# Performance work log

Hardware: AMD Instinct MI355X
Metric: run time of the kernel (lower is better)

## Reference

```python
import jax, jax.numpy as jnp
import numpy as np

B, NC, CN, K, DN = 2, 256, 256, 16, 64
G, HM, HS, HMOD, MOD_OUT = 8, 128, 128, 64, 5


def setup_inputs() -> dict:
    rng = np.random.default_rng(0)
    # per-neuron top-K neighbors within cell, excluding self, sorted (matches torch buffer build)
    scores = rng.random((NC, CN, CN)).astype(np.float32)
    ii = np.arange(CN)
    scores[:, ii, ii] = -np.inf
    conn = np.argpartition(-scores, K, axis=-1)[..., :K]
    conn = np.sort(conn, axis=-1).astype(np.int32)  # [NC, CN, K]

    key = jax.random.key(0)
    ks = jax.random.split(key, 12)
    n = lambda k, s, sc=1.0: jax.random.normal(k, s, jnp.float32) * sc
    return {
        'h': n(ks[0], (B, NC, CN, DN), 0.01),
        'w_conn': n(ks[1], (B, NC, CN, K), 0.1),
        'cell_context': n(ks[2], (B, NC, DN), 0.1),
        'neuron_id': n(ks[3], (NC, CN, DN), 0.02),
        'msg_w1': n(ks[4], (G, HM, 3 * DN), 0.05), 'msg_b1': jnp.zeros((G, HM)),
        'msg_w2': n(ks[5], (G, DN, HM), 0.005), 'msg_b2': jnp.zeros((G, DN)),
        'state_w1': n(ks[6], (G, HS, 3 * DN), 0.05), 'state_b1': jnp.zeros((G, HS)),
        'state_w2': n(ks[7], (G, DN, HS), 0.005), 'state_b2': jnp.zeros((G, DN)),
        'mod_w1': n(ks[8], (NC, 2 * DN, HMOD), 0.05), 'mod_b1': jnp.zeros((NC, HMOD)),
        'mod_w2': n(ks[9], (NC, HMOD, MOD_OUT), 0.0005), 'mod_b2': jnp.zeros((NC, MOD_OUT)),
        'conn_idx': jnp.asarray(conn),
        'cell_to_group': (jnp.arange(NC) % G).astype(jnp.int32),
    }


def reference(h, w_conn, cell_context, neuron_id,
              msg_w1, msg_b1, msg_w2, msg_b2,
              state_w1, state_b1, state_w2, state_b2,
              mod_w1, mod_b1, mod_w2, mod_b2,
              conn_idx, cell_to_group):
    nc = h.shape[1]
    cell_ix = jnp.arange(nc)[:, None, None]
    # gather K-neighbor states per neuron: [B, NC, CN, K, DN]
    nb = jax.vmap(lambda hb: hb[cell_ix, conn_idx])(h)
    # connection-weighted aggregation
    agg = jnp.einsum('bnck,bnckd->bncd', w_conn, nb)

    g = cell_to_group  # [NC]
    # grouped message MLP (2-layer), per-cell weights gathered from group table
    mfeat = jnp.concatenate([h, agg, jnp.broadcast_to(neuron_id[None], h.shape)], axis=-1)
    mh = jax.nn.gelu(jnp.einsum('bncf,nhf->bnch', mfeat, msg_w1[g]) + msg_b1[g][None, :, None, :])
    msg = jnp.einsum('bnch,ndh->bncd', mh, msg_w2[g]) + msg_b2[g][None, :, None, :]

    # grouped state MLP, residual update on h
    ctx = jnp.broadcast_to(cell_context[:, :, None, :], h.shape)
    sfeat = jnp.concatenate([h, msg, ctx], axis=-1)
    sh = jax.nn.gelu(jnp.einsum('bncf,nhf->bnch', sfeat, state_w1[g]) + state_b1[g][None, :, None, :])
    h_new = h + jnp.einsum('bnch,ndh->bncd', sh, state_w2[g]) + state_b2[g][None, :, None, :]

    # per-cell modulation MLP on pooled stats (h_mean || msg_mean)
    pooled = jnp.concatenate([h_new.mean(axis=2), msg.mean(axis=2)], axis=-1)  # [B, NC, 2DN]
    ph = jax.nn.gelu(jnp.einsum('bnf,nfh->bnh', pooled, mod_w1) + mod_b1[None])
    mod = jnp.einsum('bnh,nho->bno', ph, mod_w2) + mod_b2[None]
    return h_new, msg, mod
```

## Files before the change

kernel.cpp:

```cpp
#include <hip/hip_runtime.h>

#define B_   2
#define NC_  256
#define CN_  256
#define K_   16
#define DN_  64
#define G_   8
#define HM_  128
#define F3_  192

typedef unsigned short u16;
typedef short v8s __attribute__((ext_vector_type(8)));
typedef float v4f __attribute__((ext_vector_type(4)));

#define SMEM_BYTES 150144


__device__ __forceinline__ u16 f2b(float f) {
    unsigned v; __builtin_memcpy(&v, &f, 4);
    v = v + 0x7fffu + ((v >> 16) & 1u);
    return (u16)(v >> 16);
}
__device__ __forceinline__ v8s cvt8(const float* p) {
    float4 a = *(const float4*)p, b = *(const float4*)(p + 4);
    v8s r;
    r[0] = (short)f2b(a.x); r[1] = (short)f2b(a.y); r[2] = (short)f2b(a.z); r[3] = (short)f2b(a.w);
    r[4] = (short)f2b(b.x); r[5] = (short)f2b(b.y); r[6] = (short)f2b(b.z); r[7] = (short)f2b(b.w);
    return r;
}
__device__ __forceinline__ float gelu_t(float x) {
    float u = x * x;
    float t = 1.5957691216057308f * x * __builtin_fmaf(0.044715f, u, 1.0f);
    float e = __expf(-t);
    return x * __builtin_amdgcn_rcpf(1.0f + e);
}

__global__ __launch_bounds__(256) void cvt_w(
    const float* __restrict__ mw1, const float* __restrict__ mw2,
    const float* __restrict__ sw1, const float* __restrict__ sw2,
    u16* __restrict__ dst)
{
    int e = (blockIdx.x * 256 + threadIdx.x) * 4;
    const float* s; int off;
    if      (e < 196608) { s = mw1; off = e; }
    else if (e < 262144) { s = mw2; off = e - 196608; }
    else if (e < 458752) { s = sw1; off = e - 262144; }
    else                 { s = sw2; off = e - 458752; }
    float4 v = *(const float4*)(s + off);
    ushort4 o4;
    o4.x = f2b(v.x); o4.y = f2b(v.y); o4.z = f2b(v.z); o4.w = f2b(v.w);
    *(ushort4*)(dst + e) = o4;
}

__global__ __launch_bounds__(256) void mg_main(
    const float* __restrict__ h,    const float* __restrict__ wconn,
    const float* __restrict__ ctx,  const float* __restrict__ nid,
    const u16* __restrict__ mw1b,   const float* __restrict__ mb1,
    const u16* __restrict__ mw2b,   const float* __restrict__ mb2,
    const u16* __restrict__ sw1b,   const float* __restrict__ sb1,
    const u16* __restrict__ sw2b,   const float* __restrict__ sb2,
    const int* __restrict__ conn,   const int* __restrict__ c2g,
    const float* __restrict__ dw1,  const float* __restrict__ db1,
    const float* __restrict__ dw2,  const float* __restrict__ db2,
    float* __restrict__ outf)
{
    const int bn   = blockIdx.x;
    const int n    = bn & 255;
    const int tid  = threadIdx.x;
    const int wave = tid >> 6;
    const int lane = tid & 63;
    const int q    = lane >> 4;
    const int ln   = lane & 15;
    const int g    = c2g[n];

    extern __shared__ char smem[];
    u16*   hT   = (u16*)(smem);
    u16*   big  = (u16*)(smem + 34816);
    u16*   wg   = big;
    u16*   am   = (u16*)(smem + 104448);
    u16*   ctxl = (u16*)(smem + 141312);
    float* hsum = (float*)(smem + 141440);
    float* msum = (float*)(smem + 145536);
    float* pool = (float*)(smem + 149632);

    const size_t hbase = (size_t)bn * (CN_ * DN_);
    const size_t nbase = (size_t)n  * (CN_ * DN_);
    float* oH = outf + (size_t)bn * 16384;
    float* oM = outf + (size_t)8388608 + (size_t)bn * 16384;

    if (tid < 64) ctxl[tid] = f2b(ctx[(size_t)bn * DN_ + tid]);
    {
        const float* hrow = h + hbase + (size_t)tid * DN_;
#pragma unroll
        for (int i = 0; i < 16; ++i) {
            float4 v = *(const float4*)(hrow + i * 4);
            hT[(i * 4 + 0) * 272 + tid] = f2b(v.x);
            hT[(i * 4 + 1) * 272 + tid] = f2b(v.y);
            hT[(i * 4 + 2) * 272 + tid] = f2b(v.z);
            hT[(i * 4 + 3) * 272 + tid] = f2b(v.w);
        }
    }
    __syncthreads();

    for (int s = 0; s < 4; ++s) {
#pragma unroll
        for (int i = 0; i < 9; ++i) {
            int idx = tid + i * 256;
            if (idx < 2176) ((uint4*)wg)[idx] = make_uint4(0u, 0u, 0u, 0u);
        }
        __syncthreads();
#pragma unroll
        for (int i = 0; i < 4; ++i) {
            int p  = i * 256 + tid;
            int cl = p >> 4;
            int iv = conn[n * 4096 + s * 1024 + p];
            float wv = wconn[(size_t)bn * 4096 + s * 1024 + p];
            wg[cl * 272 + iv] = f2b(wv);
        }
        __syncthreads();
        {
            v4f a0 = {0,0,0,0}, a1 = {0,0,0,0}, a2 = {0,0,0,0}, a3 = {0,0,0,0};
            const u16* arow = wg + (wave * 16 + ln) * 272 + q * 8;
#pragma unroll
            for (int ks = 0; ks < 8; ++ks) {
                v8s a   = *(const v8s*)(arow + ks * 32);
                v8s bb0 = *(const v8s*)(hT + ( 0 + ln) * 272 + ks * 32 + q * 8);
                v8s bb1 = *(const v8s*)(hT + (16 + ln) * 272 + ks * 32 + q * 8);
                v8s bb2 = *(const v8s*)(hT + (32 + ln) * 272 + ks * 32 + q * 8);
                v8s bb3 = *(const v8s*)(hT + (48 + ln) * 272 + ks * 32 + q * 8);
                a0 = __builtin_amdgcn_mfma_f32_16x16x32_bf16(a, bb0, a0, 0, 0, 0);
                a1 = __builtin_amdgcn_mfma_f32_16x16x32_bf16(a, bb1, a1, 0, 0, 0);
                a2 = __builtin_amdgcn_mfma_f32_16x16x32_bf16(a, bb2, a2, 0, 0, 0);
                a3 = __builtin_amdgcn_mfma_f32_16x16x32_bf16(a, bb3, a3, 0, 0, 0);
            }
            int crow = s * 64 + wave * 16 + q * 4;
#pragma unroll
            for (int r = 0; r < 4; ++r) {
                am[(crow + r) * 72 +  0 + ln] = f2b(a0[r]);
                am[(crow + r) * 72 + 16 + ln] = f2b(a1[r]);
                am[(crow + r) * 72 + 32 + ln] = f2b(a2[r]);
                am[(crow + r) * 72 + 48 + ln] = f2b(a3[r]);
            }
        }
        __syncthreads();
    }

    const int cbase = wave * 64;

    {
        v8s afr[4][6];
#pragma unroll
        for (int mi = 0; mi < 4; ++mi) {
            int c = cbase + mi * 16 + ln;
            afr[mi][0] = cvt8(h + hbase + (size_t)c * 64 +  0 + q * 8);
            afr[mi][1] = cvt8(h + hbase + (size_t)c * 64 + 32 + q * 8);
            afr[mi][2] = *(const v8s*)(am + c * 72 +  0 + q * 8);
            afr[mi][3] = *(const v8s*)(am + c * 72 + 32 + q * 8);
            afr[mi][4] = cvt8(nid + nbase + (size_t)c * 64 +  0 + q * 8);
            afr[mi][5] = cvt8(nid + nbase + (size_t)c * 64 + 32 + q * 8);
        }
        float b1v[8];
#pragma unroll
        for (int nt = 0; nt < 8; ++nt) b1v[nt] = mb1[g * HM_ + nt * 16 + ln];
        const u16* w1g = mw1b + (size_t)g * HM_ * F3_;
#pragma unroll
        for (int nt = 0; nt < 8; ++nt) {
            v4f acc[4] = {{0,0,0,0},{0,0,0,0},{0,0,0,0},{0,0,0,0}};
#pragma unroll
            for (int ks = 0; ks < 6; ++ks) {
                v8s bf = *(const v8s*)(w1g + (nt * 16 + ln) * F3_ + ks * 32 + q * 8);
#pragma unroll
                for (int mi = 0; mi < 4; ++mi)
                    acc[mi] = __builtin_amdgcn_mfma_f32_16x16x32_bf16(afr[mi][ks], bf, acc[mi], 0, 0, 0);
            }
#pragma unroll
            for (int mi = 0; mi < 4; ++mi) {
                int c = cbase + mi * 16 + q * 4;
#pragma unroll
                for (int r = 0; r < 4; ++r)
                    big[(c + r) * 136 + nt * 16 + ln] = f2b(gelu_t(acc[mi][r] + b1v[nt]));
            }
        }
    }

    {
        v8s afr[4][4];
#pragma unroll
        for (int mi = 0; mi < 4; ++mi) {
            int c = cbase + mi * 16 + ln;
#pragma unroll
            for (int ks = 0; ks < 4; ++ks)
                afr[mi][ks] = *(const v8s*)(big + c * 136 + ks * 32 + q * 8);
        }
        const u16* w2g = mw2b + (size_t)g * DN_ * HM_;
        float mpart[4];
#pragma unroll
        for (int nt = 0; nt < 4; ++nt) {
            float bb = mb2[g * DN_ + nt * 16 + ln];
            v4f acc[4] = {{0,0,0,0},{0,0,0,0},{0,0,0,0},{0,0,0,0}};
#pragma unroll
            for (int ks = 0; ks < 4; ++ks) {
                v8s bf = *(const v8s*)(w2g + (nt * 16 + ln) * HM_ + ks * 32 + q * 8);
#pragma unroll
                for (int mi = 0; mi < 4; ++mi)
                    acc[mi] = __builtin_amdgcn_mfma_f32_16x16x32_bf16(afr[mi][ks], bf, acc[mi], 0, 0, 0);
            }
            float ms = 0.0f;
            int d = nt * 16 + ln;
#pragma unroll
            for (int mi = 0; mi < 4; ++mi) {
                int c = cbase + mi * 16 + q * 4;
#pragma unroll
                for (int r = 0; r < 4; ++r) {
                    float mv = acc[mi][r] + bb;
                    am[(c + r) * 72 + d] = f2b(mv);
                    oM[(size_t)(c + r) * 64 + d] = mv;
                    ms += mv;
                }
            }
            mpart[nt] = ms;
        }
#pragma unroll
        for (int nt = 0; nt < 4; ++nt)
            msum[(wave * 4 + q) * 64 + nt * 16 + ln] = mpart[nt];
    }

    {
        v8s cfr0 = *(const v8s*)(ctxl +  0 + q * 8);
        v8s cfr1 = *(const v8s*)(ctxl + 32 + q * 8);
        v8s afr[4][4];
#pragma unroll
        for (int mi = 0; mi < 4; ++mi) {
            int c = cbase + mi * 16 + ln;
            afr[mi][0] = cvt8(h + hbase + (size_t)c * 64 +  0 + q * 8);
            afr[mi][1] = cvt8(h + hbase + (size_t)c * 64 + 32 + q * 8);
            afr[mi][2] = *(const v8s*)(am + c * 72 +  0 + q * 8);
            afr[mi][3] = *(const v8s*)(am + c * 72 + 32 + q * 8);
        }
        float b1v[8];
#pragma unroll
        for (int nt = 0; nt < 8; ++nt) b1v[nt] = sb1[g * HM_ + nt * 16 + ln];
        const u16* w1g = sw1b + (size_t)g * HM_ * F3_;
#pragma unroll
        for (int nt = 0; nt < 8; ++nt) {
            v4f acc[4] = {{0,0,0,0},{0,0,0,0},{0,0,0,0},{0,0,0,0}};
#pragma unroll
            for (int ks = 0; ks < 4; ++ks) {
                v8s bf = *(const v8s*)(w1g + (nt * 16 + ln) * F3_ + ks * 32 + q * 8);
#pragma unroll
                for (int mi = 0; mi < 4; ++mi)
                    acc[mi] = __builtin_amdgcn_mfma_f32_16x16x32_bf16(afr[mi][ks], bf, acc[mi], 0, 0, 0);
            }
#pragma unroll
            for (int ks = 4; ks < 6; ++ks) {
                v8s bf = *(const v8s*)(w1g + (nt * 16 + ln) * F3_ + ks * 32 + q * 8);
                v8s aa = (ks == 4) ? cfr0 : cfr1;
#pragma unroll
                for (int mi = 0; mi < 4; ++mi)
                    acc[mi] = __builtin_amdgcn_mfma_f32_16x16x32_bf16(aa, bf, acc[mi], 0, 0, 0);
            }
#pragma unroll
            for (int mi = 0; mi < 4; ++mi) {
                int c = cbase + mi * 16 + q * 4;
#pragma unroll
                for (int r = 0; r < 4; ++r)
                    big[(c + r) * 136 + nt * 16 + ln] = f2b(gelu_t(acc[mi][r] + b1v[nt]));
            }
        }
    }

    {
        v8s afr[4][4];
#pragma unroll
        for (int mi = 0; mi < 4; ++mi) {
            int c = cbase + mi * 16 + ln;
#pragma unroll
            for (int ks = 0; ks < 4; ++ks)
                afr[mi][ks] = *(const v8s*)(big + c * 136 + ks * 32 + q * 8);
        }
        const u16* w2g = sw2b + (size_t)g * DN_ * HM_;
        float hpart[4];
#pragma unroll
        for (int nt = 0; nt < 4; ++nt) {
            float bb = sb2[g * DN_ + nt * 16 + ln];
            v4f acc[4] = {{0,0,0,0},{0,0,0,0},{0,0,0,0},{0,0,0,0}};
#pragma unroll
            for (int ks = 0; ks < 4; ++ks) {
                v8s bf = *(const v8s*)(w2g + (nt * 16 + ln) * HM_ + ks * 32 + q * 8);
#pragma unroll
                for (int mi = 0; mi < 4; ++mi)
                    acc[mi] = __builtin_amdgcn_mfma_f32_16x16x32_bf16(afr[mi][ks], bf, acc[mi], 0, 0, 0);
            }
            float hs = 0.0f;
            int d = nt * 16 + ln;
#pragma unroll
            for (int mi = 0; mi < 4; ++mi) {
                int c = cbase + mi * 16 + q * 4;
#pragma unroll
                for (int r = 0; r < 4; ++r) {
                    float hv = h[hbase + (size_t)(c + r) * 64 + d];
                    float hn = hv + acc[mi][r] + bb;
                    oH[(size_t)(c + r) * 64 + d] = hn;
                    hs += hn;
                }
            }
            hpart[nt] = hs;
        }
#pragma unroll
        for (int nt = 0; nt < 4; ++nt)
            hsum[(wave * 4 + q) * 64 + nt * 16 + ln] = hpart[nt];
    }
    __syncthreads();

    if (tid < 128) {
        int col = tid & 63;
        const float* src = (tid < 64) ? hsum : msum;
        float s = 0.0f;
#pragma unroll
        for (int i = 0; i < 16; ++i) s += src[i * 64 + col];
        pool[tid] = s * (1.0f / 256.0f);
    }
    __syncthreads();

    {
        const int col = tid & 63, fh = tid >> 6;
        const float* w1p = dw1 + ((size_t)n * 128 + fh * 32) * 64 + col;
        const float* pv  = pool + fh * 32;
        float acc = 0.0f;
#pragma unroll
        for (int f = 0; f < 32; ++f)
            acc = __builtin_fmaf(pv[f], w1p[(size_t)f * 64], acc);
        hsum[fh * 64 + col] = acc;
    }
    __syncthreads();

    if (tid < 64) {
        float a  = hsum[tid] + hsum[64 + tid] + hsum[128 + tid] + hsum[192 + tid]
                 + db1[n * 64 + tid];
        float ph = gelu_t(a);
        float part[5];
#pragma unroll
        for (int o = 0; o < 5; ++o) part[o] = ph * dw2[((size_t)n * 64 + tid) * 5 + o];
#pragma unroll
        for (int off = 32; off > 0; off >>= 1)
#pragma unroll
            for (int o = 0; o < 5; ++o) part[o] += __shfl_down(part[o], off);
        if (tid == 0) {
#pragma unroll
            for (int o = 0; o < 5; ++o)
                outf[(size_t)16777216 + bn * 5 + o] = part[o] + db2[n * 5 + o];
        }
    }
}

extern "C" void kernel_launch(void* const* d_in, const int* in_sizes, int n_in,
                              void* d_out, int out_size, void* d_ws, size_t ws_size,
                              hipStream_t stream) {
    const float* h     = (const float*)d_in[0];
    const float* wconn = (const float*)d_in[1];
    const float* ctx   = (const float*)d_in[2];
    const float* nid   = (const float*)d_in[3];
    const float* mw1   = (const float*)d_in[4];
    const float* mb1   = (const float*)d_in[5];
    const float* mw2   = (const float*)d_in[6];
    const float* mb2   = (const float*)d_in[7];
    const float* sw1   = (const float*)d_in[8];
    const float* sb1   = (const float*)d_in[9];
    const float* sw2   = (const float*)d_in[10];
    const float* sb2   = (const float*)d_in[11];
    const float* dw1   = (const float*)d_in[12];
    const float* db1   = (const float*)d_in[13];
    const float* dw2   = (const float*)d_in[14];
    const float* db2   = (const float*)d_in[15];
    const int* conn    = (const int*)d_in[16];
    const int* c2g     = (const int*)d_in[17];
    float* outf  = (float*)d_out;
    u16*   wb    = (u16*)d_ws;

    hipFuncSetAttribute(reinterpret_cast<const void*>(&mg_main),
                        hipFuncAttributeMaxDynamicSharedMemorySize, SMEM_BYTES);

    cvt_w<<<512, 256, 0, stream>>>(mw1, mw2, sw1, sw2, wb);
    mg_main<<<512, 256, SMEM_BYTES, stream>>>(h, wconn, ctx, nid,
                                              wb,           mb1,
                                              wb + 196608,  mb2,
                                              wb + 262144,  sb1,
                                              wb + 458752,  sb2,
                                              conn, c2g,
                                              dw1, db1, dw2, db2,
                                              outf);
}
```

Measured before the change: 232.5 us.

## Double block size to 512 threads, processing two aggregation stages concurrently

```diff
diff --git a/kernel.cpp b/kernel.cpp
--- a/kernel.cpp
+++ b/kernel.cpp
@@ -13,7 +13,7 @@
 typedef short v8s __attribute__((ext_vector_type(8)));
 typedef float v4f __attribute__((ext_vector_type(4)));
 
-#define SMEM_BYTES 150144
+#define SMEM_BYTES 158336
 
 
 __device__ __forceinline__ u16 f2b(float f) {
@@ -52,7 +52,7 @@
     *(ushort4*)(dst + e) = o4;
 }
 
-__global__ __launch_bounds__(256) void mg_main(
+__global__ __launch_bounds__(512) void mg_main(
     const float* __restrict__ h,    const float* __restrict__ wconn,
     const float* __restrict__ ctx,  const float* __restrict__ nid,
     const u16* __restrict__ mw1b,   const float* __restrict__ mb1,
@@ -76,12 +76,11 @@
     extern __shared__ char smem[];
     u16*   hT   = (u16*)(smem);
     u16*   big  = (u16*)(smem + 34816);
-    u16*   wg   = big;
     u16*   am   = (u16*)(smem + 104448);
     u16*   ctxl = (u16*)(smem + 141312);
     float* hsum = (float*)(smem + 141440);
-    float* msum = (float*)(smem + 145536);
-    float* pool = (float*)(smem + 149632);
+    float* msum = (float*)(smem + 149632);
+    float* pool = (float*)(smem + 157824);
 
     const size_t hbase = (size_t)bn * (CN_ * DN_);
     const size_t nbase = (size_t)n  * (CN_ * DN_);
@@ -90,67 +89,78 @@
 
     if (tid < 64) ctxl[tid] = f2b(ctx[(size_t)bn * DN_ + tid]);
     {
-        const float* hrow = h + hbase + (size_t)tid * DN_;
-#pragma unroll
-        for (int i = 0; i < 16; ++i) {
+        const int row  = tid & 255;
+        const int half = tid >> 8;
+        const float* hrow = h + hbase + (size_t)row * DN_ + half * 32;
+#pragma unroll
+        for (int i = 0; i < 8; ++i) {
             float4 v = *(const float4*)(hrow + i * 4);
-            hT[(i * 4 + 0) * 272 + tid] = f2b(v.x);
-            hT[(i * 4 + 1) * 272 + tid] = f2b(v.y);
-            hT[(i * 4 + 2) * 272 + tid] = f2b(v.z);
-            hT[(i * 4 + 3) * 272 + tid] = f2b(v.w);
+            int d0 = half * 32 + i * 4;
+            hT[(d0 + 0) * 272 + row] = f2b(v.x);
+            hT[(d0 + 1) * 272 + row] = f2b(v.y);
+            hT[(d0 + 2) * 272 + row] = f2b(v.z);
+            hT[(d0 + 3) * 272 + row] = f2b(v.w);
         }
     }
     __syncthreads();
 
-    for (int s = 0; s < 4; ++s) {
-#pragma unroll
-        for (int i = 0; i < 9; ++i) {
-            int idx = tid + i * 256;
-            if (idx < 2176) ((uint4*)wg)[idx] = make_uint4(0u, 0u, 0u, 0u);
-        }
-        __syncthreads();
-#pragma unroll
-        for (int i = 0; i < 4; ++i) {
-            int p  = i * 256 + tid;
-            int cl = p >> 4;
-            int iv = conn[n * 4096 + s * 1024 + p];
-            float wv = wconn[(size_t)bn * 4096 + s * 1024 + p];
-            wg[cl * 272 + iv] = f2b(wv);
-        }
-        __syncthreads();
-        {
-            v4f a0 = {0,0,0,0}, a1 = {0,0,0,0}, a2 = {0,0,0,0}, a3 = {0,0,0,0};
-            const u16* arow = wg + (wave * 16 + ln) * 272 + q * 8;
-#pragma unroll
-            for (int ks = 0; ks < 8; ++ks) {
-                v8s a   = *(const v8s*)(arow + ks * 32);
-                v8s bb0 = *(const v8s*)(hT + ( 0 + ln) * 272 + ks * 32 + q * 8);
-                v8s bb1 = *(const v8s*)(hT + (16 + ln) * 272 + ks * 32 + q * 8);
-                v8s bb2 = *(const v8s*)(hT + (32 + ln) * 272 + ks * 32 + q * 8);
-                v8s bb3 = *(const v8s*)(hT + (48 + ln) * 272 + ks * 32 + q * 8);
-                a0 = __builtin_amdgcn_mfma_f32_16x16x32_bf16(a, bb0, a0, 0, 0, 0);
-                a1 = __builtin_amdgcn_mfma_f32_16x16x32_bf16(a, bb1, a1, 0, 0, 0);
-                a2 = __builtin_amdgcn_mfma_f32_16x16x32_bf16(a, bb2, a2, 0, 0, 0);
-                a3 = __builtin_amdgcn_mfma_f32_16x16x32_bf16(a, bb3, a3, 0, 0, 0);
-            }
-            int crow = s * 64 + wave * 16 + q * 4;
-#pragma unroll
-            for (int r = 0; r < 4; ++r) {
-                am[(crow + r) * 72 +  0 + ln] = f2b(a0[r]);
-                am[(crow + r) * 72 + 16 + ln] = f2b(a1[r]);
-                am[(crow + r) * 72 + 32 + ln] = f2b(a2[r]);
-                am[(crow + r) * 72 + 48 + ln] = f2b(a3[r]);
-            }
-        }
-        __syncthreads();
-    }
-
-    const int cbase = wave * 64;
-
-    {
-        v8s afr[4][6];
-#pragma unroll
-        for (int mi = 0; mi < 4; ++mi) {
+    {
+        const int sg   = wave >> 2;
+        const int wl   = wave & 3;
+        const int gtid = tid & 255;
+        u16* wgg = (u16*)(smem + 34816 + sg * 34816);
+
+        for (int s = 0; s < 4; s += 2) {
+            const int st = s + sg;
+#pragma unroll
+            for (int i = 0; i < 9; ++i) {
+                int idx = gtid + i * 256;
+                if (idx < 2176) ((uint4*)wgg)[idx] = make_uint4(0u, 0u, 0u, 0u);
+            }
+            __syncthreads();
+#pragma unroll
+            for (int i = 0; i < 4; ++i) {
+                int p  = i * 256 + gtid;
+                int cl = p >> 4;
+                int iv = conn[n * 4096 + st * 1024 + p];
+                float wv = wconn[(size_t)bn * 4096 + st * 1024 + p];
+                wgg[cl * 272 + iv] = f2b(wv);
+            }
+            __syncthreads();
+            {
+                v4f a0 = {0,0,0,0}, a1 = {0,0,0,0}, a2 = {0,0,0,0}, a3 = {0,0,0,0};
+                const u16* arow = wgg + (wl * 16 + ln) * 272 + q * 8;
+#pragma unroll
+                for (int ks = 0; ks < 8; ++ks) {
+                    v8s a   = *(const v8s*)(arow + ks * 32);
+                    v8s bb0 = *(const v8s*)(hT + ( 0 + ln) * 272 + ks * 32 + q * 8);
+                    v8s bb1 = *(const v8s*)(hT + (16 + ln) * 272 + ks * 32 + q * 8);
+                    v8s bb2 = *(const v8s*)(hT + (32 + ln) * 272 + ks * 32 + q * 8);
+                    v8s bb3 = *(const v8s*)(hT + (48 + ln) * 272 + ks * 32 + q * 8);
+                    a0 = __builtin_amdgcn_mfma_f32_16x16x32_bf16(a, bb0, a0, 0, 0, 0);
+                    a1 = __builtin_amdgcn_mfma_f32_16x16x32_bf16(a, bb1, a1, 0, 0, 0);
+                    a2 = __builtin_amdgcn_mfma_f32_16x16x32_bf16(a, bb2, a2, 0, 0, 0);
+                    a3 = __builtin_amdgcn_mfma_f32_16x16x32_bf16(a, bb3, a3, 0, 0, 0);
+                }
+                int crow = st * 64 + wl * 16 + q * 4;
+#pragma unroll
+                for (int r = 0; r < 4; ++r) {
+                    am[(crow + r) * 72 +  0 + ln] = f2b(a0[r]);
+                    am[(crow + r) * 72 + 16 + ln] = f2b(a1[r]);
+                    am[(crow + r) * 72 + 32 + ln] = f2b(a2[r]);
+                    am[(crow + r) * 72 + 48 + ln] = f2b(a3[r]);
+                }
+            }
+            __syncthreads();
+        }
+    }
+
+    const int cbase = wave * 32;
+
+    {
+        v8s afr[2][6];
+#pragma unroll
+        for (int mi = 0; mi < 2; ++mi) {
             int c = cbase + mi * 16 + ln;
             afr[mi][0] = cvt8(h + hbase + (size_t)c * 64 +  0 + q * 8);
             afr[mi][1] = cvt8(h + hbase + (size_t)c * 64 + 32 + q * 8);
@@ -165,16 +175,16 @@
         const u16* w1g = mw1b + (size_t)g * HM_ * F3_;
 #pragma unroll
         for (int nt = 0; nt < 8; ++nt) {
-            v4f acc[4] = {{0,0,0,0},{0,0,0,0},{0,0,0,0},{0,0,0,0}};
+            v4f acc[2] = {{0,0,0,0},{0,0,0,0}};
 #pragma unroll
             for (int ks = 0; ks < 6; ++ks) {
                 v8s bf = *(const v8s*)(w1g + (nt * 16 + ln) * F3_ + ks * 32 + q * 8);
 #pragma unroll
-                for (int mi = 0; mi < 4; ++mi)
+                for (int mi = 0; mi < 2; ++mi)
                     acc[mi] = __builtin_amdgcn_mfma_f32_16x16x32_bf16(afr[mi][ks], bf, acc[mi], 0, 0, 0);
             }
 #pragma unroll
-            for (int mi = 0; mi < 4; ++mi) {
+            for (int mi = 0; mi < 2; ++mi) {
                 int c = cbase + mi * 16 + q * 4;
 #pragma unroll
                 for (int r = 0; r < 4; ++r)
@@ -184,9 +194,9 @@
     }
 
     {
-        v8s afr[4][4];
-#pragma unroll
-        for (int mi = 0; mi < 4; ++mi) {
+        v8s afr[2][4];
+#pragma unroll
+        for (int mi = 0; mi < 2; ++mi) {
             int c = cbase + mi * 16 + ln;
 #pragma unroll
             for (int ks = 0; ks < 4; ++ks)
@@ -197,18 +207,18 @@
 #pragma unroll
         for (int nt = 0; nt < 4; ++nt) {
             float bb = mb2[g * DN_ + nt * 16 + ln];
-            v4f acc[4] = {{0,0,0,0},{0,0,0,0},{0,0,0,0},{0,0,0,0}};
+            v4f acc[2] = {{0,0,0,0},{0,0,0,0}};
 #pragma unroll
             for (int ks = 0; ks < 4; ++ks) {
                 v8s bf = *(const v8s*)(w2g + (nt * 16 + ln) * HM_ + ks * 32 + q * 8);
 #pragma unroll
-                for (int mi = 0; mi < 4; ++mi)
+                for (int mi = 0; mi < 2; ++mi)
                     acc[mi] = __builtin_amdgcn_mfma_f32_16x16x32_bf16(afr[mi][ks], bf, acc[mi], 0, 0, 0);
             }
             float ms = 0.0f;
             int d = nt * 16 + ln;
 #pragma unroll
-            for (int mi = 0; mi < 4; ++mi) {
+            for (int mi = 0; mi < 2; ++mi) {
                 int c = cbase + mi * 16 + q * 4;
 #pragma unroll
                 for (int r = 0; r < 4; ++r) {
@@ -228,9 +238,9 @@
     {
         v8s cfr0 = *(const v8s*)(ctxl +  0 + q * 8);
         v8s cfr1 = *(const v8s*)(ctxl + 32 + q * 8);
-        v8s afr[4][4];
-#pragma unroll
-        for (int mi = 0; mi < 4; ++mi) {
+        v8s afr[2][4];
+#pragma unroll
+        for (int mi = 0; mi < 2; ++mi) {
             int c = cbase + mi * 16 + ln;
             afr[mi][0] = cvt8(h + hbase + (size_t)c * 64 +  0 + q * 8);
             afr[mi][1] = cvt8(h + hbase + (size_t)c * 64 + 32 + q * 8);
@@ -243,12 +253,12 @@
         const u16* w1g = sw1b + (size_t)g * HM_ * F3_;
 #pragma unroll
         for (int nt = 0; nt < 8; ++nt) {
-            v4f acc[4] = {{0,0,0,0},{0,0,0,0},{0,0,0,0},{0,0,0,0}};
+            v4f acc[2] = {{0,0,0,0},{0,0,0,0}};
 #pragma unroll
             for (int ks = 0; ks < 4; ++ks) {
                 v8s bf = *(const v8s*)(w1g + (nt * 16 + ln) * F3_ + ks * 32 + q * 8);
 #pragma unroll
-                for (int mi = 0; mi < 4; ++mi)
+                for (int mi = 0; mi < 2; ++mi)
                     acc[mi] = __builtin_amdgcn_mfma_f32_16x16x32_bf16(afr[mi][ks], bf, acc[mi], 0, 0, 0);
             }
 #pragma unroll
@@ -256,11 +266,11 @@
                 v8s bf = *(const v8s*)(w1g + (nt * 16 + ln) * F3_ + ks * 32 + q * 8);
                 v8s aa = (ks == 4) ? cfr0 : cfr1;
 #pragma unroll
-                for (int mi = 0; mi < 4; ++mi)
+                for (int mi = 0; mi < 2; ++mi)
                     acc[mi] = __builtin_amdgcn_mfma_f32_16x16x32_bf16(aa, bf, acc[mi], 0, 0, 0);
             }
 #pragma unroll
-            for (int mi = 0; mi < 4; ++mi) {
+            for (int mi = 0; mi < 2; ++mi) {
                 int c = cbase + mi * 16 + q * 4;
 #pragma unroll
                 for (int r = 0; r < 4; ++r)
@@ -270,9 +280,9 @@
     }
 
     {
-        v8s afr[4][4];
-#pragma unroll
-        for (int mi = 0; mi < 4; ++mi) {
+        v8s afr[2][4];
+#pragma unroll
+        for (int mi = 0; mi < 2; ++mi) {
             int c = cbase + mi * 16 + ln;
 #pragma unroll
             for (int ks = 0; ks < 4; ++ks)
@@ -283,18 +293,18 @@
 #pragma unroll
         for (int nt = 0; nt < 4; ++nt) {
             float bb = sb2[g * DN_ + nt * 16 + ln];
-            v4f acc[4] = {{0,0,0,0},{0,0,0,0},{0,0,0,0},{0,0,0,0}};
+            v4f acc[2] = {{0,0,0,0},{0,0,0,0}};
 #pragma unroll
             for (int ks = 0; ks < 4; ++ks) {
                 v8s bf = *(const v8s*)(w2g + (nt * 16 + ln) * HM_ + ks * 32 + q * 8);
 #pragma unroll
-                for (int mi = 0; mi < 4; ++mi)
+                for (int mi = 0; mi < 2; ++mi)
                     acc[mi] = __builtin_amdgcn_mfma_f32_16x16x32_bf16(afr[mi][ks], bf, acc[mi], 0, 0, 0);
             }
             float hs = 0.0f;
             int d = nt * 16 + ln;
 #pragma unroll
-            for (int mi = 0; mi < 4; ++mi) {
+            for (int mi = 0; mi < 2; ++mi) {
                 int c = cbase + mi * 16 + q * 4;
 #pragma unroll
                 for (int r = 0; r < 4; ++r) {
@@ -317,26 +327,27 @@
         const float* src = (tid < 64) ? hsum : msum;
         float s = 0.0f;
 #pragma unroll
-        for (int i = 0; i < 16; ++i) s += src[i * 64 + col];
+        for (int i = 0; i < 32; ++i) s += src[i * 64 + col];
         pool[tid] = s * (1.0f / 256.0f);
     }
     __syncthreads();
 
     {
         const int col = tid & 63, fh = tid >> 6;
-        const float* w1p = dw1 + ((size_t)n * 128 + fh * 32) * 64 + col;
-        const float* pv  = pool + fh * 32;
+        const float* w1p = dw1 + ((size_t)n * 128 + fh * 16) * 64 + col;
+        const float* pv  = pool + fh * 16;
         float acc = 0.0f;
 #pragma unroll
-        for (int f = 0; f < 32; ++f)
+        for (int f = 0; f < 16; ++f)
             acc = __builtin_fmaf(pv[f], w1p[(size_t)f * 64], acc);
         hsum[fh * 64 + col] = acc;
     }
     __syncthreads();
 
     if (tid < 64) {
-        float a  = hsum[tid] + hsum[64 + tid] + hsum[128 + tid] + hsum[192 + tid]
-                 + db1[n * 64 + tid];
+        float a = db1[n * 64 + tid];
+#pragma unroll
+        for (int j = 0; j < 8; ++j) a += hsum[j * 64 + tid];
         float ph = gelu_t(a);
         float part[5];
 #pragma unroll
@@ -381,7 +392,7 @@
                         hipFuncAttributeMaxDynamicSharedMemorySize, SMEM_BYTES);
 
     cvt_w<<<512, 256, 0, stream>>>(mw1, mw2, sw1, sw2, wb);
-    mg_main<<<512, 256, SMEM_BYTES, stream>>>(h, wconn, ctx, nid,
+    mg_main<<<512, 512, SMEM_BYTES, stream>>>(h, wconn, ctx, nid,
                                               wb,           mb1,
                                               wb + 196608,  mb2,
                                               wb + 262144,  sb1,
```

Result: no change. 235.5 us (+1.3%).
